# Optimization experiments

Hardware: AMD Instinct MI355X
Metric: run time of the kernel (lower is better)

The kernel has to match this reference:

```python
import jax, jax.numpy as jnp
import numpy as np

# dims (must match input_specs / init_kwargs)
B, N, L, D = 4, 2000, 32, 64
H, ND, K, DOUT = 4, 64, 20, 64  # num_heads, node_dim, topk, out_dim
EPS = 1e-8


def setup_inputs() -> dict:
    key = jax.random.key(0)
    ks = jax.random.split(key, 10)
    lim_emb = float(np.sqrt(6.0 / (N + ND)))  # xavier_uniform-ish for embeddings
    lim_l1 = float(np.sqrt(1.0 / H))          # torch Linear default-ish
    lim_l2 = float(np.sqrt(1.0 / (2 * H)))
    lim_w = float(np.sqrt(6.0 / (D + DOUT)))
    return {
        "x": jax.random.normal(ks[0], (B, N, L, D), dtype=jnp.float32),
        "e1": jax.random.uniform(ks[1], (H, N, ND), minval=-lim_emb, maxval=lim_emb, dtype=jnp.float32),
        "e2": jax.random.uniform(ks[2], (H, ND, N), minval=-lim_emb, maxval=lim_emb, dtype=jnp.float32),
        "temperature": jnp.ones((H,), dtype=jnp.float32),
        "ew1": jax.random.uniform(ks[3], (H, 2 * H), minval=-lim_l1, maxval=lim_l1, dtype=jnp.float32),
        "eb1": jax.random.uniform(ks[4], (2 * H,), minval=-lim_l1, maxval=lim_l1, dtype=jnp.float32),
        "ew2": jax.random.uniform(ks[5], (2 * H, 1), minval=-lim_l2, maxval=lim_l2, dtype=jnp.float32),
        "eb2": jax.random.uniform(ks[6], (1,), minval=-lim_l2, maxval=lim_l2, dtype=jnp.float32),
        "weight": jax.random.uniform(ks[7], (D, DOUT), minval=-lim_w, maxval=lim_w, dtype=jnp.float32),
        "bias": jnp.zeros((DOUT,), dtype=jnp.float32),
    }


def _graph_learner(e1, e2, temperature, ew1, eb1, ew2, eb2):
    # per-head scores: (H, N, N)
    scores = jnp.einsum("hnd,hdm->hnm", e1, e2)
    adj = jax.nn.softmax(jax.nn.relu(scores) / temperature[:, None, None], axis=-1)
    # topk sparsification along each row (dim=1 in torch == last axis here)
    _, idx = jax.lax.top_k(adj, K)  # (H, N, K)
    mask = jnp.zeros_like(adj).at[
        jnp.arange(H)[:, None, None], jnp.arange(N)[None, :, None], idx
    ].set(1.0)
    adj = adj * mask
    adj = adj / (jnp.sum(adj, axis=-1, keepdims=True) + EPS)
    # edge encoder MLP over head dim (dropout is identity in eval mode)
    feats = jnp.transpose(adj, (1, 2, 0))              # (N, N, H)
    hid = jax.nn.relu(feats @ ew1 + eb1)               # (N, N, 2H)
    ew = (hid @ ew2 + eb2)[..., 0]                     # (N, N)
    final_adj = jax.nn.sigmoid(ew) * jnp.mean(adj, axis=0)
    return final_adj, adj


def reference(x, e1, e2, temperature, ew1, eb1, ew2, eb2, weight, bias):
    final_adj, _ = _graph_learner(e1, e2, temperature, ew1, eb1, ew2, eb2)
    Bv, Nv, Lv, Dv = x.shape
    xr = jnp.transpose(x, (0, 2, 1, 3)).reshape(Bv * Lv, Nv, Dv)  # (B*L, N, D)
    support = xr @ weight                                          # (B*L, N, Dout)
    # adj.t() @ support  ->  out[b,i,:] = sum_j adj[j,i] * support[b,j,:]
    out = jnp.einsum("ji,bjd->bid", final_adj, support) + bias
    out = jnp.transpose(out.reshape(Bv, Lv, Nv, -1), (0, 2, 1, 3))  # (B, N, L, Dout)
    return out, final_adj
```

## Files before the change

### kernel.cpp

```cpp
#include <hip/hip_runtime.h>

#define NB   2000
#define HH   4
#define KK   20
#define KP   2048
#define GA   4
#define EPSF 1e-8f

typedef unsigned short ushort;
typedef unsigned long long ull;
using short8   = __attribute__((ext_vector_type(8))) short;
using floatx4  = __attribute__((ext_vector_type(4))) float;
using ushortx4 = __attribute__((ext_vector_type(4))) unsigned short;
using ushortx8 = __attribute__((ext_vector_type(8))) unsigned short;

__device__ inline ushort f2bf(float f) {
    unsigned u = __builtin_bit_cast(unsigned, f);
    u += 0x7fffu + ((u >> 16) & 1u);
    return (ushort)(u >> 16);
}

__device__ __forceinline__ void gload_lds16(const ushort* g, ushort* l) {
    __builtin_amdgcn_global_load_lds(
        (const __attribute__((address_space(1))) void*)g,
        (__attribute__((address_space(3))) void*)l, 16, 0, 0);
}

template<int CTRL>
__device__ __forceinline__ float dppmax(float x) {
    int xi = __builtin_bit_cast(int, x);
    int yi = __builtin_amdgcn_update_dpp(xi, xi, CTRL, 0xF, 0xF, false);
    return fmaxf(x, __builtin_bit_cast(float, yi));
}

__device__ __forceinline__ float wavemax63(float x) {
    x = dppmax<0x111>(x);
    x = dppmax<0x112>(x);
    x = dppmax<0x114>(x);
    x = dppmax<0x118>(x);
    x = dppmax<0x142>(x);
    x = dppmax<0x143>(x);
    return x;
}

#define COMP(v,i) ((i)==0?(v).x:(i)==1?(v).y:(i)==2?(v).z:(v).w)

__global__ __launch_bounds__(512, 4) void k_scores_topk(
    const float* __restrict__ e1, const float* __restrict__ e2,
    const float* __restrict__ temperature,
    int* __restrict__ topk_idx, float* __restrict__ topk_val)
{
    const int h  = blockIdx.y;
    const int n0 = blockIdx.x * GA;
    const int t  = threadIdx.x;
    const int w  = t >> 6, lane = t & 63;

    __shared__ float e1s[GA][64];
    __shared__ float scoresS[GA][2048];
    __shared__ float red[GA][4];
    __shared__ ull   lists[4][GA][KK + 1];
    __shared__ float selpv[GA][KK];
    __shared__ int   seli[GA][KK];
    __shared__ float ssum[GA];

    if (t < 256)
        e1s[t >> 6][t & 63] = e1[(size_t)(h * NB + n0 + (t >> 6)) * 64 + (t & 63)];
    __syncthreads();

    const float rtemp = 1.f / temperature[h];
    const float* __restrict__ e2h = e2 + (size_t)h * 64 * NB;

    {
        const int mb1 = w * 256 + lane * 4;
        const int ml1 = (mb1 < NB) ? mb1 : (NB - 4);

        float acc[GA][4];
#pragma unroll
        for (int r = 0; r < GA; r++)
#pragma unroll
            for (int c = 0; c < 4; c++) acc[r][c] = 0.f;

        for (int d4 = 0; d4 < 64; d4 += 4) {
            float4 ev0 = *(const float4*)&e1s[0][d4];
            float4 ev1 = *(const float4*)&e1s[1][d4];
            float4 ev2 = *(const float4*)&e1s[2][d4];
            float4 ev3 = *(const float4*)&e1s[3][d4];
#pragma unroll
            for (int dd = 0; dd < 4; dd++) {
                float4 a = *(const float4*)(e2h + (size_t)(d4 + dd) * NB + ml1);
                float f0 = COMP(ev0, dd), f1 = COMP(ev1, dd);
                float f2 = COMP(ev2, dd), f3 = COMP(ev3, dd);
                acc[0][0] += f0*a.x; acc[0][1] += f0*a.y; acc[0][2] += f0*a.z; acc[0][3] += f0*a.w;
                acc[1][0] += f1*a.x; acc[1][1] += f1*a.y; acc[1][2] += f1*a.z; acc[1][3] += f1*a.w;
                acc[2][0] += f2*a.x; acc[2][1] += f2*a.y; acc[2][2] += f2*a.z; acc[2][3] += f2*a.w;
                acc[3][0] += f3*a.x; acc[3][1] += f3*a.y; acc[3][2] += f3*a.z; acc[3][3] += f3*a.w;
            }
        }

#pragma unroll
        for (int r = 0; r < GA; r++) {
            float4 v; v.x = acc[r][0]; v.y = acc[r][1]; v.z = acc[r][2]; v.w = acc[r][3];
            *(float4*)&scoresS[r][mb1] = v;
        }
    }
    __syncthreads();

    if (w < 4) {
        const int  mbase = w * 512 + lane * 8;
        const bool valid = (mbase < NB);

        float acc[GA][8];
#pragma unroll
        for (int r = 0; r < GA; r++) {
            float4 lo = *(const float4*)&scoresS[r][mbase];
            float4 hi = *(const float4*)&scoresS[r][mbase + 4];
            acc[r][0] = lo.x; acc[r][1] = lo.y; acc[r][2] = lo.z; acc[r][3] = lo.w;
            acc[r][4] = hi.x; acc[r][5] = hi.y; acc[r][6] = hi.z; acc[r][7] = hi.w;
        }

#pragma unroll
        for (int r = 0; r < GA; r++) {
            float tvm = -1.f;
#pragma unroll
            for (int k = 0; k < 8; k++) {
                float v = valid ? fmaxf(acc[r][k], 0.f) * rtemp : -1.f;
                acc[r][k] = v;
                tvm = fmaxf(tvm, v);
            }
            tvm = wavemax63(tvm);
            if (lane == 63) red[r][w] = tvm;
        }

        float lm[GA]; int ak[GA];
#pragma unroll
        for (int r = 0; r < GA; r++) {
            float l = acc[r][0]; int a = 0;
#pragma unroll
            for (int k = 1; k < 8; k++)
                if (acc[r][k] > l) { l = acc[r][k]; a = k; }
            lm[r] = l; ak[r] = a;
        }

        for (int round = 0; round < KK; round++) {
            float M[GA];
#pragma unroll
            for (int r = 0; r < GA; r++) M[r] = lm[r];
#pragma unroll
            for (int r = 0; r < GA; r++) M[r] = dppmax<0x111>(M[r]);
#pragma unroll
            for (int r = 0; r < GA; r++) M[r] = dppmax<0x112>(M[r]);
#pragma unroll
            for (int r = 0; r < GA; r++) M[r] = dppmax<0x114>(M[r]);
#pragma unroll
            for (int r = 0; r < GA; r++) M[r] = dppmax<0x118>(M[r]);
#pragma unroll
            for (int r = 0; r < GA; r++) M[r] = dppmax<0x142>(M[r]);
#pragma unroll
            for (int r = 0; r < GA; r++) M[r] = dppmax<0x143>(M[r]);
#pragma unroll
            for (int r = 0; r < GA; r++)
                M[r] = __builtin_bit_cast(float,
                         __builtin_amdgcn_readlane(__builtin_bit_cast(int, M[r]), 63));
#pragma unroll
            for (int r = 0; r < GA; r++) {
                ull ball = __ballot(lm[r] == M[r]);
                int wl   = __ffsll(ball) - 1;
                if (lane == wl) {
                    int gidx = mbase + ak[r];
                    lists[w][r][round] =
                        ((ull)__float_as_uint(M[r]) << 32) | (unsigned)~gidx;
#pragma unroll
                    for (int k = 0; k < 8; k++) if (k == ak[r]) acc[r][k] = -2.f;
                    float l = acc[r][0]; int a = 0;
#pragma unroll
                    for (int k = 1; k < 8; k++)
                        if (acc[r][k] > l) { l = acc[r][k]; a = k; }
                    lm[r] = l; ak[r] = a;
                }
            }
        }
#pragma unroll
        for (int r = 0; r < GA; r++)
            if (lane == 0) lists[w][r][KK] = 0ULL;
    }
    __syncthreads();

    if (t < GA) {
        const int r = t;
        float mx = fmaxf(fmaxf(red[r][0], red[r][1]), fmaxf(red[r][2], red[r][3]));
        int p0 = 0, p1 = 0, p2 = 0, p3 = 0;
        ull h0 = lists[0][r][0], h1 = lists[1][r][0];
        ull h2 = lists[2][r][0], h3 = lists[3][r][0];
        float ss = 0.f;
        for (int q = 0; q < KK; q++) {
            ull a_ = h0 >= h1 ? h0 : h1; int wa = h0 >= h1 ? 0 : 1;
            ull b_ = h2 >= h3 ? h2 : h3; int wb = h2 >= h3 ? 2 : 3;
            ull bk = a_ >= b_ ? a_ : b_; int bw = a_ >= b_ ? wa : wb;
            float tvv = __uint_as_float((unsigned)(bk >> 32));
            float pv  = __expf(tvv - mx);
            selpv[r][q] = pv;
            seli[r][q]  = (int)~(unsigned)bk;
            ss += pv;
            if      (bw == 0) h0 = lists[0][r][++p0];
            else if (bw == 1) h1 = lists[1][r][++p1];
            else if (bw == 2) h2 = lists[2][r][++p2];
            else              h3 = lists[3][r][++p3];
        }
        ssum[r] = ss;
    }
    __syncthreads();

    if (t < GA * KK) {
        int r = t / KK, q = t % KK;
        int o = (h * NB + n0 + r) * KK + q;
        topk_idx[o] = seli[r][q];
        topk_val[o] = selpv[r][q] / (ssum[r] + EPSF);
    }
}

__global__ __launch_bounds__(256) void k_final_adj(
    const int* __restrict__ topk_idx, const float* __restrict__ topk_val,
    const float* __restrict__ ew1, const float* __restrict__ eb1,
    const float* __restrict__ ew2, const float* __restrict__ eb2,
    float* __restrict__ fadj_out, ushort* __restrict__ faT_b)
{
    const int i = blockIdx.x;
    const int t = threadIdx.x;

    __shared__ float rows[HH][NB];
    __shared__ float w1[32];
    __shared__ float b1[8];
    __shared__ float w2[8];
    __shared__ float b2v;

    for (int k = t; k < HH * NB; k += 256) ((float*)rows)[k] = 0.f;
    if (t < 32) w1[t] = ew1[t];
    if (t < 8)  { b1[t] = eb1[t]; w2[t] = ew2[t]; }
    if (t == 0) b2v = eb2[0];
    __syncthreads();

    if (t < HH * KK) {
        int h = t / KK, r = t % KK;
        int o = (h * NB + i) * KK + r;
        rows[h][topk_idx[o]] = topk_val[o];
    }
    __syncthreads();

#pragma unroll
    for (int k = 0; k < 8; k++) {
        int j = k * 256 + t;
        if (j < NB) {
            float f0 = rows[0][j], f1 = rows[1][j], f2 = rows[2][j], f3 = rows[3][j];
            float mean = (f0 + f1 + f2 + f3) * 0.25f;
            float outv = 0.f;
            if (mean > 0.f) {
                float ewv = b2v;
#pragma unroll
                for (int c = 0; c < 8; c++) {
                    float hid = f0 * w1[c] + f1 * w1[8 + c] + f2 * w1[16 + c] + f3 * w1[24 + c] + b1[c];
                    hid = fmaxf(hid, 0.f);
                    ewv += hid * w2[c];
                }
                float sig = 1.f / (1.f + expf(-ewv));
                outv = sig * mean;
                faT_b[(size_t)j * KP + i] = f2bf(outv);
            }
            fadj_out[(size_t)i * NB + j] = outv;
        }
    }
}

__global__ __launch_bounds__(256) void k_support_t(
    const float* __restrict__ x, const float* __restrict__ w,
    ushort* __restrict__ ST)
{
    const int jt = blockIdx.x;
    const int bl = blockIdx.y;
    const int b_ = bl >> 5, l = bl & 31;
    const int t  = threadIdx.x;

    __shared__ float  xs[64][65];
    __shared__ float  ws[64 * 64];
    __shared__ ushort ob[64 * 65];

    for (int k = t; k < 4096; k += 256) ws[k] = w[k];

    {
        const float* xb = x + (size_t)b_ * 4096000 + (size_t)l * 64;
#pragma unroll
        for (int p = 0; p < 4; p++) {
            int q  = p * 256 + t;
            int jl = q >> 4, f4 = q & 15;
            int jg = jt * 64 + jl;
            int jc = jg < NB ? jg : (NB - 1);
            *(float4*)&xs[jl][f4 * 4] =
                *(const float4*)(xb + (size_t)jc * 2048 + f4 * 4);
        }
    }
    __syncthreads();

    const int dq = t & 15;
    const int g  = t >> 4;
    float acc[4][4];
#pragma unroll
    for (int r = 0; r < 4; r++)
#pragma unroll
        for (int c = 0; c < 4; c++) acc[r][c] = 0.f;

    for (int dd = 0; dd < 64; dd++) {
        float4 w4 = *(const float4*)&ws[dd * 64 + dq * 4];
#pragma unroll
        for (int r = 0; r < 4; r++) {
            float xv = xs[g * 4 + r][dd];
            acc[r][0] += xv * w4.x;
            acc[r][1] += xv * w4.y;
            acc[r][2] += xv * w4.z;
            acc[r][3] += xv * w4.w;
        }
    }

#pragma unroll
    for (int r = 0; r < 4; r++) {
        int jl = g * 4 + r;
        bool jvalid = (jt * 64 + jl) < NB;
        ushort* dst = &ob[jl * 65 + dq * 4];
        dst[0] = jvalid ? f2bf(acc[r][0]) : (ushort)0;
        dst[1] = jvalid ? f2bf(acc[r][1]) : (ushort)0;
        dst[2] = jvalid ? f2bf(acc[r][2]) : (ushort)0;
        dst[3] = jvalid ? f2bf(acc[r][3]) : (ushort)0;
    }
    __syncthreads();

#pragma unroll
    for (int p = 0; p < 2; p++) {
        int q = p * 256 + t;
        int rc = q >> 3, s = q & 7;
        ushortx8 o;
#pragma unroll
        for (int k = 0; k < 8; k++) o[k] = ob[(s * 8 + k) * 65 + rc];
        *(ushortx8*)&ST[(size_t)(bl * 64 + rc) * KP + jt * 64 + s * 8] = o;
    }
}

__global__ __launch_bounds__(512, 2) void k_gemm(
    const ushort* __restrict__ A, const ushort* __restrict__ B,
    const float* __restrict__ bias, float* __restrict__ out)
{
    __shared__ ushort As[2][256 * 64];
    __shared__ ushort Bs[2][256 * 64];

    const int t    = threadIdx.x;
    const int lane = t & 63, wave = t >> 6;
    const int wm   = wave & 1;
    const int wn   = wave >> 1;

    const int lin = blockIdx.y * 8 + blockIdx.x;
    const int swz = (lin & 7) * 32 + (lin >> 3);
    const int i0  = (swz & 7) * 256;
    const int c0  = (swz >> 3) * 256;

    const int lr = lane >> 3;
    const int dg = lane & 7;

    floatx4 acc[8][4];
#pragma unroll
    for (int r = 0; r < 8; r++)
#pragma unroll
        for (int c = 0; c < 4; c++) acc[r][c] = (floatx4)(0.f);

#define STAGE(buf, kb)                                                         \
    {                                                                          \
        _Pragma("unroll")                                                      \
        for (int p = 0; p < 4; p++) {                                          \
            int rowb = wave * 32 + p * 8;                                      \
            int row  = rowb + lr;                                              \
            int g    = dg ^ lr;                                                \
            gload_lds16(&A[(size_t)(i0 + row) * KP + (kb) * 64 + g * 8],       \
                        &As[buf][rowb * 64]);                                  \
            gload_lds16(&B[(size_t)(c0 + row) * KP + (kb) * 64 + g * 8],       \
                        &Bs[buf][rowb * 64]);                                  \
        }                                                                      \
    }

    STAGE(0, 0);
    int cur = 0;

    for (int kb = 0; kb < 32; kb++) {
        if (kb < 31) {
            STAGE(cur ^ 1, kb + 1);
            asm volatile("s_waitcnt vmcnt(8)" ::: "memory");
        } else {
            asm volatile("s_waitcnt vmcnt(0)" ::: "memory");
        }
        __builtin_amdgcn_s_barrier();
        __builtin_amdgcn_sched_barrier(0);

#pragma unroll
        for (int kk = 0; kk < 2; kk++) {
            short8 af[8], bf[4];
            const int gidx = kk * 4 + (lane >> 4);
            const int dsw  = gidx ^ (lane & 7);
#pragma unroll
            for (int r = 0; r < 8; r++) {
                int m = wm * 128 + r * 16 + (lane & 15);
                af[r] = *(const short8*)&As[cur][m * 64 + dsw * 8];
            }
#pragma unroll
            for (int c = 0; c < 4; c++) {
                int m = wn * 64 + c * 16 + (lane & 15);
                bf[c] = *(const short8*)&Bs[cur][m * 64 + dsw * 8];
            }
#pragma unroll
            for (int r = 0; r < 8; r++)
#pragma unroll
                for (int c = 0; c < 4; c++)
                    acc[r][c] = __builtin_amdgcn_mfma_f32_16x16x32_bf16(af[r], bf[c], acc[r][c], 0, 0, 0);
        }

        __builtin_amdgcn_s_barrier();
        cur ^= 1;
    }
#undef STAGE

    const int mq = (lane >> 4) * 4;
    const int nn = lane & 15;
#pragma unroll
    for (int r = 0; r < 8; r++) {
#pragma unroll
        for (int c = 0; c < 4; c++) {
            int cg = c0 + wn * 64 + c * 16 + nn;
            float bv = bias[cg & 63];
            int b_ = cg >> 11, rem = cg & 2047;
            float* op = out + (size_t)b_ * 4096000 + rem;
#pragma unroll
            for (int rg = 0; rg < 4; rg++) {
                int i = i0 + wm * 128 + r * 16 + mq + rg;
                if (i < NB) op[(size_t)i * 2048] = acc[r][c][rg] + bv;
            }
        }
    }
}

extern "C" void kernel_launch(void* const* d_in, const int* in_sizes, int n_in,
                              void* d_out, int out_size, void* d_ws, size_t ws_size,
                              hipStream_t stream)
{
    const float* x           = (const float*)d_in[0];
    const float* e1          = (const float*)d_in[1];
    const float* e2          = (const float*)d_in[2];
    const float* temperature = (const float*)d_in[3];
    const float* ew1         = (const float*)d_in[4];
    const float* eb1         = (const float*)d_in[5];
    const float* ew2         = (const float*)d_in[6];
    const float* eb2         = (const float*)d_in[7];
    const float* weight      = (const float*)d_in[8];
    const float* bias        = (const float*)d_in[9];

    float* out  = (float*)d_out;
    float* fadj = out + 16384000;

    ushort* ST       = (ushort*)d_ws;
    ushort* faT_b    = ST + (size_t)8192 * KP;
    int*    topk_idx = (int*)(faT_b + (size_t)KP * KP);
    float*  topk_val = (float*)(topk_idx + 160000);

    hipMemsetAsync(faT_b, 0, (size_t)KP * KP * sizeof(ushort), stream);

    k_scores_topk<<<dim3(NB / GA, HH), 512, 0, stream>>>(e1, e2, temperature,
                                                         topk_idx, topk_val);
    k_final_adj<<<NB, 256, 0, stream>>>(topk_idx, topk_val, ew1, eb1, ew2, eb2,
                                        fadj, faT_b);
    k_support_t<<<dim3(32, 128), 256, 0, stream>>>(x, weight, ST);
    k_gemm<<<dim3(8, 32), 512, 0, stream>>>(faT_b, ST, bias, out);
}
```

Measured before the change: 361.7 us.

## Interleave global prefetch with MFMA phases in GEMM main loop

```diff
diff --git a/kernel.cpp b/kernel.cpp
--- a/kernel.cpp
+++ b/kernel.cpp
@@ -359,8 +359,11 @@
     const int i0  = (swz & 7) * 256;
     const int c0  = (swz >> 3) * 256;
 
-    const int lr = lane >> 3;
-    const int dg = lane & 7;
+    const int lr   = lane >> 3;
+    const int dg   = lane & 7;
+    const int ln15 = lane & 15;
+    const int dsw0 = ((lane >> 4) + 0) ^ (lane & 7);
+    const int dsw1 = ((lane >> 4) + 4) ^ (lane & 7);
 
     floatx4 acc[8][4];
 #pragma unroll
@@ -368,59 +371,74 @@
 #pragma unroll
         for (int c = 0; c < 4; c++) acc[r][c] = (floatx4)(0.f);
 
-#define STAGE(buf, kb)                                                         \
+#define STAGE_PAIR(buf, kb_, p_)                                               \
     {                                                                          \
-        _Pragma("unroll")                                                      \
-        for (int p = 0; p < 4; p++) {                                          \
-            int rowb = wave * 32 + p * 8;                                      \
-            int row  = rowb + lr;                                              \
-            int g    = dg ^ lr;                                                \
-            gload_lds16(&A[(size_t)(i0 + row) * KP + (kb) * 64 + g * 8],       \
-                        &As[buf][rowb * 64]);                                  \
-            gload_lds16(&B[(size_t)(c0 + row) * KP + (kb) * 64 + g * 8],       \
-                        &Bs[buf][rowb * 64]);                                  \
-        }                                                                      \
-    }
-
-    STAGE(0, 0);
-    int cur = 0;
+        int rowb = wave * 32 + (p_) * 8;                                       \
+        int row  = rowb + lr;                                                  \
+        int g    = dg ^ lr;                                                    \
+        gload_lds16(&A[(size_t)(i0 + row) * KP + (kb_) * 64 + g * 8],          \
+                    &As[buf][rowb * 64]);                                      \
+        gload_lds16(&B[(size_t)(c0 + row) * KP + (kb_) * 64 + g * 8],          \
+                    &Bs[buf][rowb * 64]);                                      \
+    }
+
+#pragma unroll
+    for (int p = 0; p < 4; p++) STAGE_PAIR(0, 0, p);
 
     for (int kb = 0; kb < 32; kb++) {
-        if (kb < 31) {
-            STAGE(cur ^ 1, kb + 1);
-            asm volatile("s_waitcnt vmcnt(8)" ::: "memory");
-        } else {
-            asm volatile("s_waitcnt vmcnt(0)" ::: "memory");
-        }
-        __builtin_amdgcn_s_barrier();
-        __builtin_amdgcn_sched_barrier(0);
-
-#pragma unroll
-        for (int kk = 0; kk < 2; kk++) {
-            short8 af[8], bf[4];
-            const int gidx = kk * 4 + (lane >> 4);
-            const int dsw  = gidx ^ (lane & 7);
-#pragma unroll
-            for (int r = 0; r < 8; r++) {
-                int m = wm * 128 + r * 16 + (lane & 15);
-                af[r] = *(const short8*)&As[cur][m * 64 + dsw * 8];
-            }
+        const int cur = kb & 1;
+        const int nxt = cur ^ 1;
+        short8 bf0[4], bf1[4];
+
+#pragma unroll
+        for (int p = 0; p < 4; p++) {
+            short8 a0k0, a0k1, a1k0, a1k1;
+            const int m0 = wm * 128 + (2 * p) * 16 + ln15;
+            const int m1 = m0 + 16;
+
+            if (p == 0) {
+                if (kb < 31) {
+                    STAGE_PAIR(nxt, kb + 1, 0);
+                    asm volatile("s_waitcnt vmcnt(2)" ::: "memory");
+                } else {
+                    asm volatile("s_waitcnt vmcnt(0)" ::: "memory");
+                }
+                __builtin_amdgcn_s_barrier();
+                __builtin_amdgcn_sched_barrier(0);
+#pragma unroll
+                for (int c = 0; c < 4; c++) {
+                    int m = wn * 64 + c * 16 + ln15;
+                    bf0[c] = *(const short8*)&Bs[cur][m * 64 + dsw0 * 8];
+                    bf1[c] = *(const short8*)&Bs[cur][m * 64 + dsw1 * 8];
+                }
+                a0k0 = *(const short8*)&As[cur][m0 * 64 + dsw0 * 8];
+                a0k1 = *(const short8*)&As[cur][m0 * 64 + dsw1 * 8];
+                a1k0 = *(const short8*)&As[cur][m1 * 64 + dsw0 * 8];
+                a1k1 = *(const short8*)&As[cur][m1 * 64 + dsw1 * 8];
+            } else {
+                a0k0 = *(const short8*)&As[cur][m0 * 64 + dsw0 * 8];
+                a0k1 = *(const short8*)&As[cur][m0 * 64 + dsw1 * 8];
+                a1k0 = *(const short8*)&As[cur][m1 * 64 + dsw0 * 8];
+                a1k1 = *(const short8*)&As[cur][m1 * 64 + dsw1 * 8];
+                if (kb < 31) STAGE_PAIR(nxt, kb + 1, p);
+                __builtin_amdgcn_s_barrier();
+            }
+
+            asm volatile("s_waitcnt lgkmcnt(0)" ::: "memory");
+            __builtin_amdgcn_sched_barrier(0);
+            __builtin_amdgcn_s_setprio(1);
 #pragma unroll
             for (int c = 0; c < 4; c++) {
-                int m = wn * 64 + c * 16 + (lane & 15);
-                bf[c] = *(const short8*)&Bs[cur][m * 64 + dsw * 8];
-            }
-#pragma unroll
-            for (int r = 0; r < 8; r++)
-#pragma unroll
-                for (int c = 0; c < 4; c++)
-                    acc[r][c] = __builtin_amdgcn_mfma_f32_16x16x32_bf16(af[r], bf[c], acc[r][c], 0, 0, 0);
-        }
-
-        __builtin_amdgcn_s_barrier();
-        cur ^= 1;
-    }
-#undef STAGE
+                acc[2 * p][c]     = __builtin_amdgcn_mfma_f32_16x16x32_bf16(a0k0, bf0[c], acc[2 * p][c], 0, 0, 0);
+                acc[2 * p][c]     = __builtin_amdgcn_mfma_f32_16x16x32_bf16(a0k1, bf1[c], acc[2 * p][c], 0, 0, 0);
+                acc[2 * p + 1][c] = __builtin_amdgcn_mfma_f32_16x16x32_bf16(a1k0, bf0[c], acc[2 * p + 1][c], 0, 0, 0);
+                acc[2 * p + 1][c] = __builtin_amdgcn_mfma_f32_16x16x32_bf16(a1k1, bf1[c], acc[2 * p + 1][c], 0, 0, 0);
+            }
+            __builtin_amdgcn_s_setprio(0);
+            __builtin_amdgcn_s_barrier();
+        }
+    }
+#undef STAGE_PAIR
 
     const int mq = (lane >> 4) * 4;
     const int nn = lane & 15;
```

Result: no change. 366.8 us (+1.4%).
